# Optimization experiments

Hardware: AMD Instinct MI355X
Metric: run time of the kernel (lower is better)

The kernel has to match this reference:

```python
import jax, jax.numpy as jnp
import numpy as np
from jax import lax

M_BLOCKS = 4
D = 768
N = 8
L = 2040  # divisible by 1,2,3,4 so every block is full, matching the floor-based slicing


def setup_inputs() -> dict:
    key = jax.random.key(0)
    ks = jax.random.split(key, 7)
    X = jax.random.normal(ks[0], (N, L, D), dtype=jnp.float32)
    # char_mixer: Conv1d(d, d, kernel_size=3, padding='same')
    conv_w = jax.random.normal(ks[1], (D, D, 3), dtype=jnp.float32) * (1.0 / np.sqrt(3 * D))
    conv_b = jax.random.normal(ks[2], (D,), dtype=jnp.float32) * 0.01
    # F_R: Linear(d, 1)
    wr = jax.random.normal(ks[3], (D, 1), dtype=jnp.float32) * (1.0 / np.sqrt(D))
    br = jax.random.normal(ks[4], (1,), dtype=jnp.float32) * 0.01
    # F_D: Linear(d, d)
    wd = jax.random.normal(ks[5], (D, D), dtype=jnp.float32) * (1.0 / np.sqrt(D))
    bd = jax.random.normal(ks[6], (D,), dtype=jnp.float32) * 0.01
    return {"X": X, "conv_w": conv_w, "conv_b": conv_b, "wr": wr, "br": br, "wd": wd, "bd": bd}


def reference(X, conv_w, conv_b, wr, br, wd, bd):
    n, l, d = X.shape
    # char mixer: Conv1d over sequence (NCH layout)
    x = lax.conv_general_dilated(
        X.transpose(0, 2, 1), conv_w, window_strides=(1,), padding='SAME',
        dimension_numbers=('NCH', 'OIH', 'NCH'))
    x = (x + conv_b[None, :, None]).transpose(0, 2, 1)  # (N, L, d)

    # multi-scale block-pooled candidates X_B: (N, L, M, d)
    cands = []
    for b in range(1, M_BLOCKS + 1):  # small fixed loop over block sizes
        xb = x.reshape(n, l // b, b, d).mean(axis=2)       # mean-pool F over each block
        cands.append(jnp.repeat(xb, b, axis=1))            # broadcast block mean to positions
    XB = jnp.stack(cands, axis=2)

    # route scores F_R: Linear(d,1); softmax over trailing size-1 dim (faithful to source)
    P = jax.nn.softmax(XB @ wr + br, axis=-1)              # (N, L, M, 1)

    # calibration: softmax(P P^T) P
    P = P.reshape(n, l, M_BLOCKS)
    A = jax.nn.softmax(jnp.einsum('nlm,nkm->nlk', P, P), axis=-1)  # (N, L, L)
    P = jnp.einsum('nlk,nkm->nlm', A, P)                   # (N, L, M)

    # blend candidates and project with F_D
    X_hat = jnp.einsum('nlm,nlmd->nld', P, XB)             # (N, L, d)
    return X_hat @ wd + bd
```

## Files before the change

kernel.cpp:

```cpp
#include <hip/hip_runtime.h>

#define N_B    8
#define L_SEQ  2040
#define D_DIM  768
#define KDIM   2304
#define M_ROWS 16320
#define LPAD   2042

typedef __bf16 bf16x8 __attribute__((ext_vector_type(8)));
typedef float  f32x4  __attribute__((ext_vector_type(4)));

__device__ __forceinline__ unsigned short f2bf_u(float f) {
  union { float f; unsigned u; } v; v.f = f;
  unsigned u = v.u;
  return (unsigned short)((u + 0x7FFFu + ((u >> 16) & 1u)) >> 16);
}

__device__ __forceinline__ void async16(const unsigned short* g, const unsigned char* l) {
  __builtin_amdgcn_global_load_lds(
      (const __attribute__((address_space(1))) void*)g,
      (__attribute__((address_space(3))) void*)l, 16, 0, 0);
}

__global__ void k_pad(const float* __restrict__ X, unsigned short* __restrict__ Xpad) {
  size_t idx = ((size_t)blockIdx.x * 256 + threadIdx.x) * 4;
  const size_t per_n = (size_t)LPAD * D_DIM;
  int n = (int)(idx / per_n);
  size_t rem = idx - (size_t)n * per_n;
  int lp = (int)(rem / D_DIM);
  int d  = (int)(rem - (size_t)lp * D_DIM);
  ushort4 o;
  if (lp == 0 || lp == LPAD - 1) {
    o.x = 0; o.y = 0; o.z = 0; o.w = 0;
  } else {
    const float4 f = *(const float4*)&X[((size_t)n * L_SEQ + (lp - 1)) * D_DIM + d];
    o.x = f2bf_u(f.x); o.y = f2bf_u(f.y); o.z = f2bf_u(f.z); o.w = f2bf_u(f.w);
  }
  *(ushort4*)&Xpad[idx] = o;
}

__global__ void k_tr2(const float* __restrict__ wd, unsigned short* __restrict__ wdT,
                      const float* __restrict__ cw, unsigned short* __restrict__ cwT) {
  __shared__ float tile[32][33];
  const int z = blockIdx.z;
  const float* in = z ? cw : wd;
  unsigned short* out = z ? cwT : wdT;
  const int R = 768, C = z ? 2304 : 768;
  if (!z && blockIdx.x >= 24) return;
  int tx = threadIdx.x, ty = threadIdx.y;
  int c0 = blockIdx.x * 32;
  int r0 = blockIdx.y * 32;
  for (int i = ty; i < 32; i += 8) {
    int r = r0 + i, c = c0 + tx;
    tile[i][tx] = (r < R && c < C) ? in[(size_t)r * C + c] : 0.f;
  }
  __syncthreads();
  for (int i = ty; i < 32; i += 8) {
    int oc = c0 + i;
    int orr = r0 + tx;
    if (oc < C && orr < R) out[(size_t)oc * R + orr] = f2bf_u(tile[tx][i]);
  }
}

__global__ __launch_bounds__(256) void k_w2b(
    const unsigned short* __restrict__ wdT, const unsigned short* __restrict__ cwT,
    unsigned short* __restrict__ Bblk,
    const float* __restrict__ conv_b, const float* __restrict__ wd,
    const float* __restrict__ bd, float* __restrict__ bias2) {
  __shared__ unsigned short sA[128 * 32];
  __shared__ unsigned short sB[128 * 32];
  __shared__ float red[256];
  const int bid = blockIdx.x;
  const int t = threadIdx.x;

  if (bid >= 108) {
    const int b2 = bid - 108;
    const int o = b2 * 64 + (t & 63);
    const int sl = t >> 6;
    float acc = 0.f;
    for (int dm = sl * 192; dm < sl * 192 + 192; ++dm)
      acc += conv_b[dm] * wd[(size_t)dm * D_DIM + o];
    red[t] = acc;
    __syncthreads();
    if (t < 64)
      bias2[o] = 4.f * (red[t] + red[t + 64] + red[t + 128] + red[t + 192]) + bd[o];
    return;
  }

  const int bm = bid / 18, bn = bid - bm * 18;
  const int lane = t & 63, w = t >> 6;
  const int wr = w >> 1, wc = w & 1;
  const int lr = lane & 15, lg = lane >> 4;

  const int c0 = t, c1 = t + 256;
  const unsigned short* aB0 = wdT + (size_t)(bm * 128 + (c0 >> 2)) * 768 + (c0 & 3) * 8;
  const unsigned short* aB1 = wdT + (size_t)(bm * 128 + (c1 >> 2)) * 768 + (c1 & 3) * 8;
  const unsigned short* bB0 = cwT + (size_t)(bn * 128 + (c0 >> 2)) * 768 + (c0 & 3) * 8;
  const unsigned short* bB1 = cwT + (size_t)(bn * 128 + (c1 >> 2)) * 768 + (c1 & 3) * 8;

  f32x4 acc[4][4] = {};
  int aOff[4], bOff[4];
#pragma unroll
  for (int i = 0; i < 4; ++i) {
    aOff[i] = (wr * 64 + i * 16 + lr) * 4 + lg;
    bOff[i] = (wc * 64 + i * 16 + lr) * 4 + lg;
  }
  const bf16x8* At = (const bf16x8*)sA;
  const bf16x8* Bt = (const bf16x8*)sB;

  for (int kt = 0; kt < 24; ++kt) {
    const int ko = kt * 32;
    __syncthreads();
    async16(aB0 + ko, (const unsigned char*)&sA[c0 * 8]);
    async16(aB1 + ko, (const unsigned char*)&sA[c1 * 8]);
    async16(bB0 + ko, (const unsigned char*)&sB[c0 * 8]);
    async16(bB1 + ko, (const unsigned char*)&sB[c1 * 8]);
    __syncthreads();
    bf16x8 av[4], bv[4];
#pragma unroll
    for (int i = 0; i < 4; ++i) { av[i] = At[aOff[i]]; bv[i] = Bt[bOff[i]]; }
#pragma unroll
    for (int mi = 0; mi < 4; ++mi)
#pragma unroll
      for (int ni = 0; ni < 4; ++ni)
        acc[mi][ni] = __builtin_amdgcn_mfma_f32_16x16x32_bf16(av[mi], bv[ni], acc[mi][ni], 0, 0, 0);
  }

#pragma unroll
  for (int ni = 0; ni < 4; ++ni) {
    const int jp = bn * 128 + wc * 64 + ni * 16 + lr;
    const int di = jp / 3;
    const int kk = jp - di * 3;
    const int j = kk * 768 + di;
    const int kt2 = j >> 6, rem = j & 63;
    const int kh = rem >> 5, o = (rem >> 3) & 3, e = rem & 7;
    const size_t jbase = (size_t)kt2 * 16384 + kh * 8192 + o * 128 + e;
#pragma unroll
    for (int mi = 0; mi < 4; ++mi) {
      const int row0 = bm * 128 + wr * 64 + mi * 16 + lg * 4;
      f32x4 v = acc[mi][ni];
#pragma unroll
      for (int i = 0; i < 4; ++i) {
        const int dd = row0 + i;
        const int p = dd >> 8, cl = dd & 255, blk = cl >> 4, r = cl & 15;
        Bblk[(size_t)p * 589824 + jbase + blk * 512 + r * 8] = f2bf_u(v[i]);
      }
    }
  }
}

__global__ __launch_bounds__(512, 2) void k_conv192(
    const unsigned short* __restrict__ Xpad, const unsigned short* __restrict__ Bblk,
    const float* __restrict__ bias2, float* __restrict__ Y) {
  __shared__ unsigned char lds[114688];

  const int tid = threadIdx.x;
  const int lane = tid & 63;
  const int wid = tid >> 6;
  const int wr = wid >> 2, wc = wid & 3;

  const int bid = blockIdx.x;
  const int xcd = bid & 7, idx = bid >> 3;
  const int swz = (xcd < 7 ? xcd * 32 : 224 + (xcd - 7) * 31) + idx;
  const int bm = swz / 3, bn = swz - bm * 3;

  const unsigned short *aS0, *aS1, *aS2;
  {
#define ACHUNK(rr, dst) { \
    int c = tid + (rr) * 512; \
    int kh = c / 768, q = c - kh * 768; \
    int li = q & 63; \
    int rl = (q >> 6) * 16 + (li & 15); \
    int m = bm * 192 + rl; \
    int n = m / L_SEQ, l = m - n * L_SEQ; \
    dst = Xpad + (size_t)(n * LPAD + l) * D_DIM + kh * 32 + (li >> 4) * 8; }
    ACHUNK(0, aS0) ACHUNK(1, aS1) ACHUNK(2, aS2)
#undef ACHUNK
  }
  const unsigned short* bS = Bblk + (size_t)bn * 589824 + tid * 8;
  const int dA0 = tid * 16, dA1 = dA0 + 8192, dA2 = dA0 + 16384;
  const int dB0 = 24576 + tid * 16, dB1 = dB0 + 8192, dB2 = dB0 + 16384, dB3 = dB0 + 24576;

  const int aRd0 = wr * 6144 + lane * 16;
  const int bRd0 = 24576 + wc * 4096 + lane * 16;

  f32x4 acc[6][4] = {};
  bf16x8 av[6], bv[4];

#define STG(src, koff, dst) async16((src) + (koff), lds + nbb + (dst))
#define LD_A(kh) \
    _Pragma("unroll") \
    for (int mi = 0; mi < 6; ++mi) \
      av[mi] = *(const bf16x8*)(lds + cb + aRd0 + (kh) * 12288 + mi * 1024);
#define LD_B(kh) \
    _Pragma("unroll") \
    for (int ni = 0; ni < 4; ++ni) \
      bv[ni] = *(const bf16x8*)(lds + cb + bRd0 + (kh) * 16384 + (ni) * 1024);
#define MF24 \
    __builtin_amdgcn_s_setprio(1); \
    _Pragma("unroll") \
    for (int mi = 0; mi < 6; ++mi) \
      _Pragma("unroll") \
      for (int ni = 0; ni < 4; ++ni) \
        acc[mi][ni] = __builtin_amdgcn_mfma_f32_16x16x32_bf16(av[mi], bv[ni], acc[mi][ni], 0, 0, 0); \
    __builtin_amdgcn_s_setprio(0);

  {
    const int nbb = 0;
    STG(aS0, 0, dA0); STG(aS1, 0, dA1); STG(aS2, 0, dA2);
    STG(bS, 0, dB0);  STG(bS, 4096, dB1); STG(bS, 8192, dB2); STG(bS, 12288, dB3);
  }
  __syncthreads();

  for (int t = 0; t < 36; ++t) {
    const int cb = (t & 1) * 57344;
    const int nbb = ((t & 1) ^ 1) * 57344;
    const bool st = (t < 35);
    const int aoff = (t + 1) * 64;
    const size_t boff = (size_t)(t + 1) * 16384;

    LD_A(0); LD_B(0);
    if (st) {
      STG(aS0, aoff, dA0); STG(aS1, aoff, dA1);
      STG(bS, boff, dB0);  STG(bS, boff + 4096, dB1);
    }
    MF24;
    LD_A(1); LD_B(1);
    if (st) {
      STG(aS2, aoff, dA2);
      STG(bS, boff + 8192, dB2); STG(bS, boff + 12288, dB3);
    }
    MF24;
    __syncthreads();
  }

  const int lr = lane & 15, lg = lane >> 4;
  const f32x4 bias = *(const f32x4*)&bias2[bn * 256 + lane * 4];
#pragma unroll
  for (int p = 0; p < 2; ++p) {
    if (p) __syncthreads();
    if (wr == p) {
#pragma unroll
      for (int mi = 0; mi < 6; ++mi)
#pragma unroll
        for (int ni = 0; ni < 4; ++ni)
#pragma unroll
          for (int i = 0; i < 4; ++i)
            *(float*)(lds + ((mi * 16 + lg * 4 + i) * 256 + (wc * 64 + ni * 16 + lr)) * 4) =
                acc[mi][ni][i];
    }
    __syncthreads();
    f32x4 y[12];
#pragma unroll
    for (int i = 0; i < 12; ++i)
      y[i] = *(const f32x4*)(lds + ((wid * 12 + i) * 256 + lane * 4) * 4);
    f32x4 m2[6], m3[4], m4[3];
#pragma unroll
    for (int j = 0; j < 6; ++j) m2[j] = (y[2 * j] + y[2 * j + 1]) * 0.5f;
#pragma unroll
    for (int j = 0; j < 4; ++j) m3[j] = (y[3 * j] + y[3 * j + 1] + y[3 * j + 2]) * (1.f / 3.f);
#pragma unroll
    for (int j = 0; j < 3; ++j) m4[j] = (y[4 * j] + y[4 * j + 1] + y[4 * j + 2] + y[4 * j + 3]) * 0.25f;
    const int grow0 = bm * 192 + p * 96 + wid * 12;
#pragma unroll
    for (int i = 0; i < 12; ++i) {
      f32x4 o = y[i] + m2[i >> 1] + m3[i / 3] + m4[i >> 2] + bias;
      *(f32x4*)&Y[(size_t)(grow0 + i) * D_DIM + bn * 256 + lane * 4] = o;
    }
  }
#undef STG
#undef LD_A
#undef LD_B
#undef MF24
}

extern "C" void kernel_launch(void* const* d_in, const int* in_sizes, int n_in,
                              void* d_out, int out_size, void* d_ws, size_t ws_size,
                              hipStream_t stream) {
  const float* X      = (const float*)d_in[0];
  const float* conv_w = (const float*)d_in[1];
  const float* conv_b = (const float*)d_in[2];
  const float* wd     = (const float*)d_in[5];
  const float* bd     = (const float*)d_in[6];
  float* out = (float*)d_out;

  const size_t off_Xpad  = 0;
  const size_t off_wdT   = 25092096;
  const size_t off_cwT   = 26271744;
  const size_t off_Bblk  = 29810688;
  const size_t off_bias2 = 33349632;
  const size_t NEED      = 33352704;
  if (ws_size < NEED) return;

  char* ws = (char*)d_ws;
  unsigned short* Xpad  = (unsigned short*)(ws + off_Xpad);
  unsigned short* wdT   = (unsigned short*)(ws + off_wdT);
  unsigned short* cwT   = (unsigned short*)(ws + off_cwT);
  unsigned short* Bblk  = (unsigned short*)(ws + off_Bblk);
  float*          bias2 = (float*)(ws + off_bias2);

  k_pad<<<12252, 256, 0, stream>>>(X, Xpad);
  k_tr2<<<dim3(72, 24, 2), dim3(32, 8), 0, stream>>>(wd, wdT, conv_w, cwT);
  k_w2b<<<120, 256, 0, stream>>>(wdT, cwT, Bblk, conv_b, wd, bd, bias2);
  k_conv192<<<255, 512, 0, stream>>>(Xpad, Bblk, bias2, out);
}
```

Measured before the change: 102.0 us.

## Load conv GEMM B fragments directly from global into registers, bypassing LDS

The B (weight) operand is no longer staged through shared memory. Each wave now loads its B fragments straight from the pre-blocked global layout into two register banks, with the next half-step's bank prefetched during the current MFMAs. LDS shrinks to hold only double-buffered A tiles, which frees shared memory and removes the B async copies and LDS reads. The cost is that each of the two wave rows fetches the same B data from global/L2 separately, and global load latency is exposed if the prefetch distance is too short.

Measured after the change: 113.1 us. +10.9%, slower.

```diff
diff --git a/kernel.cpp b/kernel.cpp
--- a/kernel.cpp
+++ b/kernel.cpp
@@ -152,7 +152,7 @@
 __global__ __launch_bounds__(512, 2) void k_conv192(
     const unsigned short* __restrict__ Xpad, const unsigned short* __restrict__ Bblk,
     const float* __restrict__ bias2, float* __restrict__ Y) {
-  __shared__ unsigned char lds[114688];
+  __shared__ unsigned char lds[98304];
 
   const int tid = threadIdx.x;
   const int lane = tid & 63;
@@ -177,60 +177,59 @@
     ACHUNK(0, aS0) ACHUNK(1, aS1) ACHUNK(2, aS2)
 #undef ACHUNK
   }
-  const unsigned short* bS = Bblk + (size_t)bn * 589824 + tid * 8;
   const int dA0 = tid * 16, dA1 = dA0 + 8192, dA2 = dA0 + 16384;
-  const int dB0 = 24576 + tid * 16, dB1 = dB0 + 8192, dB2 = dB0 + 16384, dB3 = dB0 + 24576;
 
   const int aRd0 = wr * 6144 + lane * 16;
-  const int bRd0 = 24576 + wc * 4096 + lane * 16;
+
+  const unsigned short* bF0 = Bblk + (size_t)bn * 589824 + (wc * 4 + 0) * 512 + lane * 8;
+  const unsigned short* bF1 = bF0 + 512;
+  const unsigned short* bF2 = bF0 + 1024;
+  const unsigned short* bF3 = bF0 + 1536;
 
   f32x4 acc[6][4] = {};
-  bf16x8 av[6], bv[4];
+  bf16x8 av[6], bP[4], bQ[4];
 
 #define STG(src, koff, dst) async16((src) + (koff), lds + nbb + (dst))
 #define LD_A(kh) \
     _Pragma("unroll") \
     for (int mi = 0; mi < 6; ++mi) \
       av[mi] = *(const bf16x8*)(lds + cb + aRd0 + (kh) * 12288 + mi * 1024);
-#define LD_B(kh) \
-    _Pragma("unroll") \
-    for (int ni = 0; ni < 4; ++ni) \
-      bv[ni] = *(const bf16x8*)(lds + cb + bRd0 + (kh) * 16384 + (ni) * 1024);
-#define MF24 \
+#define LD_B(bank, off) \
+    bank[0] = *(const bf16x8*)(bF0 + (off)); \
+    bank[1] = *(const bf16x8*)(bF1 + (off)); \
+    bank[2] = *(const bf16x8*)(bF2 + (off)); \
+    bank[3] = *(const bf16x8*)(bF3 + (off));
+#define MF24(bank) \
     __builtin_amdgcn_s_setprio(1); \
     _Pragma("unroll") \
     for (int mi = 0; mi < 6; ++mi) \
       _Pragma("unroll") \
       for (int ni = 0; ni < 4; ++ni) \
-        acc[mi][ni] = __builtin_amdgcn_mfma_f32_16x16x32_bf16(av[mi], bv[ni], acc[mi][ni], 0, 0, 0); \
+        acc[mi][ni] = __builtin_amdgcn_mfma_f32_16x16x32_bf16(av[mi], bank[ni], acc[mi][ni], 0, 0, 0); \
     __builtin_amdgcn_s_setprio(0);
 
   {
     const int nbb = 0;
     STG(aS0, 0, dA0); STG(aS1, 0, dA1); STG(aS2, 0, dA2);
-    STG(bS, 0, dB0);  STG(bS, 4096, dB1); STG(bS, 8192, dB2); STG(bS, 12288, dB3);
-  }
+  }
+  LD_B(bP, 0);
   __syncthreads();
 
   for (int t = 0; t < 36; ++t) {
-    const int cb = (t & 1) * 57344;
-    const int nbb = ((t & 1) ^ 1) * 57344;
+    const int cb = (t & 1) * 24576;
+    const int nbb = ((t & 1) ^ 1) * 24576;
     const bool st = (t < 35);
     const int aoff = (t + 1) * 64;
-    const size_t boff = (size_t)(t + 1) * 16384;
-
-    LD_A(0); LD_B(0);
-    if (st) {
-      STG(aS0, aoff, dA0); STG(aS1, aoff, dA1);
-      STG(bS, boff, dB0);  STG(bS, boff + 4096, dB1);
-    }
-    MF24;
-    LD_A(1); LD_B(1);
-    if (st) {
-      STG(aS2, aoff, dA2);
-      STG(bS, boff + 8192, dB2); STG(bS, boff + 12288, dB3);
-    }
-    MF24;
+    const size_t bo1 = (size_t)t * 16384 + 8192;
+    const size_t bo0 = (size_t)(t + 1) * 16384;
+
+    if (st) { STG(aS0, aoff, dA0); STG(aS1, aoff, dA1); STG(aS2, aoff, dA2); }
+    LD_B(bQ, bo1);
+    LD_A(0);
+    MF24(bP);
+    if (st) { LD_B(bP, bo0); }
+    LD_A(1);
+    MF24(bQ);
     __syncthreads();
   }
 
```
